# Kernel tuning notes

Measured on AMD Instinct MI355X. Metric: run time of the kernel, lower is better.

Reference implementation:

```python
import jax, jax.numpy as jnp
import numpy as np

EPS = 1e-12  # F.normalize default eps


def _unfold3(x):
    # torch F.unfold(kernel=3, padding=1): [B,C,H,W] -> [B, C*9, H*W],
    # patch elements ordered (c, kh, kw), locations row-major.
    B, C, H, W = x.shape
    xp = jnp.pad(x, ((0, 0), (0, 0), (1, 1), (1, 1)))
    patches = jnp.stack([xp[:, :, i:i + H, j:j + W]
                         for i in range(3) for j in range(3)], axis=2)  # [B,C,9,H,W]
    return patches.reshape(B, C * 9, H * W)


def _fold3(u, H, W):
    # torch F.fold(kernel=3, padding=1): sum of overlapping patches.
    B, CK, L = u.shape
    C = CK // 9
    p = u.reshape(B, C, 3, 3, H, W)
    out = jnp.zeros((B, C, H + 2, W + 2), u.dtype)
    for i in range(3):
        for j in range(3):
            out = out.at[:, :, i:i + H, j:j + W].add(p[:, :, i, j])
    return out[:, :, 1:H + 1, 1:W + 1]


def _l2norm(x, axis):
    n = jnp.sqrt(jnp.sum(x * x, axis=axis, keepdims=True))
    return x / jnp.maximum(n, EPS)


def setup_inputs() -> dict:
    key = jax.random.key(0)
    k1, k2, k3 = jax.random.split(key, 3)
    shape = (4, 256, 64, 64)
    return {
        "feature_current": jax.random.normal(k1, shape, dtype=jnp.float32),
        "feature_refer": jax.random.normal(k2, shape, dtype=jnp.float32),
        "feature_refer_blur": jax.random.normal(k3, shape, dtype=jnp.float32),
    }


def reference(feature_current, feature_refer, feature_refer_blur):
    B, C, H, W = feature_current.shape
    cu = _unfold3(feature_current)                      # [B, C*9, L]
    ru = _unfold3(feature_refer)                        # [B, C*9, L]
    rbu = jnp.transpose(_unfold3(feature_refer_blur), (0, 2, 1))  # [B, L, C*9]
    rbu = _l2norm(rbu, axis=2)
    cu_n = _l2norm(cu, axis=1)
    # cosine similarity between every refer-blur patch and every current patch
    rel = jnp.einsum('bld,bdm->blm', rbu, cu_n)         # [B, L, L]
    max_index = jnp.argmax(rel, axis=1)                 # [B, L] best refer patch per current loc
    # gather matched sharp-reference patches (index broadcast over patch dim)
    matched = jnp.take_along_axis(ru, max_index[:, None, :], axis=2)  # [B, C*9, L]
    folded = _fold3(matched, H, W)                      # [B, C, H, W]
    return feature_current + folded
```

## Files before the change

kernel.cpp:

```cpp
#include <hip/hip_runtime.h>
#include <hip/hip_bf16.h>
#include <stdint.h>

#define HW 4096
#define C_ 256
#define B_ 4

static const size_t CHW = (size_t)C_ * HW;

typedef _Float16 f16;
typedef f16 f16x8 __attribute__((ext_vector_type(8)));
typedef float f32x4 __attribute__((ext_vector_type(4)));

__device__ __forceinline__ unsigned long long pack_key(float v, int i) {
    unsigned u = __float_as_uint(v);
    u = (u & 0x80000000u) ? ~u : (u | 0x80000000u);
    return ((unsigned long long)u << 32) | (unsigned long long)(0xFFFFFFFFu - (unsigned)i);
}

__global__ __launch_bounds__(256) void sqsum_kernel(const float* __restrict__ frb,
                                                    float* __restrict__ sbuf) {
    int b = blockIdx.x;
    int ij = blockIdx.y * 256 + threadIdx.x;
    int g = blockIdx.z;
    const float* p = frb + (size_t)b * CHW + (size_t)g * 32 * HW + ij;
    float s = 0.f;
#pragma unroll 8
    for (int c = 0; c < 32; ++c) {
        float v = p[(size_t)c * HW];
        s = fmaf(v, v, s);
    }
    sbuf[((size_t)b * 8 + g) * HW + ij] = s;
}

__global__ __launch_bounds__(256) void invn_kernel(const float* __restrict__ sbuf,
                                                   float* __restrict__ invn) {
    int b = blockIdx.x;
    int l = blockIdx.y * 256 + threadIdx.x;
    int lh = l >> 6, lw = l & 63;
    float s = 0.f;
#pragma unroll
    for (int dh = -1; dh <= 1; ++dh) {
        int h = lh + dh;
        if ((unsigned)h >= 64u) continue;
#pragma unroll
        for (int dw = -1; dw <= 1; ++dw) {
            int w = lw + dw;
            if ((unsigned)w >= 64u) continue;
            float t = 0.f;
#pragma unroll
            for (int g = 0; g < 8; ++g)
                t += sbuf[((size_t)b * 8 + g) * HW + h * 64 + w];
            s += t;
        }
    }
    float n = sqrtf(s);
    invn[b * HW + l] = 1.0f / fmaxf(n, 1e-12f);
}

__global__ __launch_bounds__(256) void conv_kernel(const float* __restrict__ fcB,
                                                   const float* __restrict__ frbB,
                                                   f16* __restrict__ AB) {
    int zz = blockIdx.z;
    int b = zz >> 1;
    const float* src = ((zz & 1) ? frbB : fcB) + (size_t)b * CHW;
    f16* dst = AB + (size_t)b * 4194304 + (size_t)(zz & 1) * 2097152;
    __shared__ float T[64][65];
    int m0 = blockIdx.x * 64, k0 = blockIdx.y * 64;
    int t = threadIdx.x;
    int kl = t >> 4, mq = (t & 15) * 4;
#pragma unroll
    for (int it = 0; it < 4; ++it) {
        float4 v = *reinterpret_cast<const float4*>(src + (size_t)(k0 + kl + it * 16) * HW + m0 + mq);
        T[kl + it * 16][mq + 0] = v.x;
        T[kl + it * 16][mq + 1] = v.y;
        T[kl + it * 16][mq + 2] = v.z;
        T[kl + it * 16][mq + 3] = v.w;
    }
    __syncthreads();
    int ml = t >> 2, kc = (t & 3) * 16;
    f16x8 h0, h1, lo0, lo1;
#pragma unroll
    for (int j = 0; j < 8; ++j) {
        float a = T[kc + j][ml];
        f16 h = (f16)a;
        h0[j] = h;
        lo0[j] = (f16)(a - (float)h);
        float a2 = T[kc + 8 + j][ml];
        f16 h2 = (f16)a2;
        h1[j] = h2;
        lo1[j] = (f16)(a2 - (float)h2);
    }
    size_t base = (size_t)(m0 + ml) * 512 + k0 + kc;
    *reinterpret_cast<f16x8*>(dst + base) = h0;
    *reinterpret_cast<f16x8*>(dst + base + 8) = h1;
    *reinterpret_cast<f16x8*>(dst + base + 256) = lo0;
    *reinterpret_cast<f16x8*>(dst + base + 264) = lo1;
}

__global__ __launch_bounds__(256, 4) void gram_mfma_kernel(const f16* __restrict__ ABbase,
                                                           float* __restrict__ Gbase) {
    const f16* Af = ABbase + (size_t)blockIdx.z * 4194304;
    const f16* Bf = Af + 2097152;
    float* G = Gbase + (size_t)blockIdx.z * ((size_t)HW * HW);
    __shared__ char Asb[2][16384];
    __shared__ char Bsb[2][16384];
    int tid = threadIdx.x;
    int lane = tid & 63;
    int wave = tid >> 6;
    int wr = wave >> 1, wc = wave & 1;

    int id = blockIdx.y * gridDim.x + blockIdx.x;
    int xcd = id & 7, local = id >> 3;
    int bx = (xcd & 1) * 16 + (local & 15);
    int by = (xcd >> 1) * 8 + (local >> 4);
    int m0 = by * 128, l0 = bx * 128;
    f32x4 acc[4][4] = {};

    int mB = tid >> 3;
    int sw = ((tid & 7) ^ (mB & 7)) << 4;
    const char* gaA0 = (const char*)Af + (size_t)(m0 + mB) * 1024 + sw;
    const char* gaB0 = (const char*)Bf + (size_t)(l0 + mB) * 1024 + sw;
    char* ldA = &Asb[0][0] + (tid & ~63) * 16;
    char* ldB = &Bsb[0][0] + (tid & ~63) * 16;

    unsigned aoff[4], boff[4], choff[2];
#pragma unroll
    for (int q = 0; q < 4; ++q) {
        aoff[q] = (unsigned)((wr * 64 + q * 16 + (lane & 15)) * 128);
        boff[q] = (unsigned)((wc * 64 + q * 16 + (lane & 15)) * 128);
    }
#pragma unroll
    for (int kk = 0; kk < 2; ++kk)
        choff[kk] = (unsigned)((((kk * 4) + (lane >> 4)) ^ (lane & 7)) << 4);

    const int akbArr[12] = {0, 128, 256, 384, 512, 640, 768, 896, 0, 128, 256, 384};
    const int bkbArr[12] = {0, 128, 256, 384, 0, 128, 256, 384, 512, 640, 768, 896};

#define STAGE_TILE(buf, akb, bkb)                                                      \
    {                                                                                  \
        _Pragma("unroll")                                                              \
        for (int i = 0; i < 4; ++i) {                                                  \
            __builtin_amdgcn_global_load_lds(                                          \
                (const __attribute__((address_space(1))) uint32_t*)(gaA0 + i * 32768 + (akb)), \
                (__attribute__((address_space(3))) uint32_t*)(ldA + (buf) * 16384 + i * 4096), \
                16, 0, 0);                                                             \
            __builtin_amdgcn_global_load_lds(                                          \
                (const __attribute__((address_space(1))) uint32_t*)(gaB0 + i * 32768 + (bkb)), \
                (__attribute__((address_space(3))) uint32_t*)(ldB + (buf) * 16384 + i * 4096), \
                16, 0, 0);                                                             \
        }                                                                              \
    }

    STAGE_TILE(0, akbArr[0], bkbArr[0]);
    asm volatile("s_waitcnt vmcnt(0)" ::: "memory");
    __builtin_amdgcn_s_barrier();

#pragma unroll
    for (int t = 0; t < 12; ++t) {
        const int cur = t & 1;
        if (t < 11) STAGE_TILE(cur ^ 1, akbArr[t + 1], bkbArr[t + 1]);
#pragma unroll
        for (int kk = 0; kk < 2; ++kk) {
            f16x8 av[4], bv[4];
#pragma unroll
            for (int q = 0; q < 4; ++q) {
                av[q] = *reinterpret_cast<const f16x8*>(&Asb[cur][0] + aoff[q] + choff[kk]);
                bv[q] = *reinterpret_cast<const f16x8*>(&Bsb[cur][0] + boff[q] + choff[kk]);
            }
#pragma unroll
            for (int mi = 0; mi < 4; ++mi)
#pragma unroll
                for (int ni = 0; ni < 4; ++ni)
                    acc[mi][ni] = __builtin_amdgcn_mfma_f32_16x16x32_f16(
                        av[mi], bv[ni], acc[mi][ni], 0, 0, 0);
        }
        asm volatile("s_waitcnt vmcnt(0)" ::: "memory");
        __builtin_amdgcn_s_barrier();
    }
#undef STAGE_TILE

#pragma unroll
    for (int mi = 0; mi < 4; ++mi) {
#pragma unroll
        for (int ni = 0; ni < 4; ++ni) {
            int n = l0 + wc * 64 + ni * 16 + (lane & 15);
            int mr = m0 + wr * 64 + mi * 16 + (lane >> 4) * 4;
#pragma unroll
            for (int r = 0; r < 4; ++r)
                G[(size_t)(mr + r) * HW + n] = acc[mi][ni][r];
        }
    }
}

#define TBK 32
__global__ __launch_bounds__(256) void gram_kernel(const float* __restrict__ Amat,
                                                   const float* __restrict__ Bmat,
                                                   float* __restrict__ G,
                                                   int l_start, int CWP) {
    __shared__ float As[TBK][128];
    __shared__ float Bs[TBK][128];
    int m0 = blockIdx.y * 128;
    int l0g = l_start + blockIdx.x * 128;
    bool inrange = (l0g >= 0 && l0g < HW);
    int tid = threadIdx.x;
    int tx = tid & 15;
    int ty = tid >> 4;
    float acc[8][8] = {};

    if (inrange) {
        for (int k0 = 0; k0 < C_; k0 += TBK) {
#pragma unroll
            for (int it = 0; it < 4; ++it) {
                int idx = tid + it * 256;
                int r = idx >> 5;
                int c4 = idx & 31;
                float4 av = *reinterpret_cast<const float4*>(Amat + (size_t)(k0 + r) * HW + m0 + c4 * 4);
                *reinterpret_cast<float4*>(&As[r][c4 * 4]) = av;
                float4 bv = *reinterpret_cast<const float4*>(Bmat + (size_t)(k0 + r) * HW + l0g + c4 * 4);
                *reinterpret_cast<float4*>(&Bs[r][c4 * 4]) = bv;
            }
            __syncthreads();
#pragma unroll
            for (int k = 0; k < TBK; ++k) {
                float a[8], bb[8];
                *(float4*)&a[0] = *(float4*)&As[k][ty * 8];
                *(float4*)&a[4] = *(float4*)&As[k][ty * 8 + 4];
                *(float4*)&bb[0] = *(float4*)&Bs[k][tx * 8];
                *(float4*)&bb[4] = *(float4*)&Bs[k][tx * 8 + 4];
#pragma unroll
                for (int i = 0; i < 8; ++i)
#pragma unroll
                    for (int j = 0; j < 8; ++j)
                        acc[i][j] = fmaf(a[i], bb[j], acc[i][j]);
            }
            __syncthreads();
        }
    }
#pragma unroll
    for (int i = 0; i < 8; ++i) {
        int m = m0 + ty * 8 + i;
        float* row = G + (size_t)m * CWP + blockIdx.x * 128 + tx * 8;
        *(float4*)row = *(float4*)&acc[i][0];
        *(float4*)(row + 4) = *(float4*)&acc[i][4];
    }
}

__global__ __launch_bounds__(512, 4) void argmax3_kernel(const float* __restrict__ Gbase,
                                                         const float* __restrict__ invnB,
                                                         unsigned long long* __restrict__ keysB) {
    const float* G = Gbase + (size_t)blockIdx.z * ((size_t)HW * HW);
    const float* invn = invnB + (size_t)blockIdx.z * HW;
    unsigned long long* keys = keysB + (size_t)blockIdx.z * HW;

    int id = blockIdx.y * gridDim.x + blockIdx.x;
    int xcd = id & 7, pos = id >> 3;
    int mh = xcd * 8 + (pos >> 3);
    int c0 = (pos & 7) * 8;

    int lane = threadIdx.x & 63;
    int wave = threadIdx.x >> 6;
    int mwb = wave * 8;

    bool laneUp = lane >= 1, laneDn = lane <= 62;
    bool mhUp = mh >= 1, mhDn = mh <= 62;

    unsigned rowOff[3][10];
    int br0 = max(mh - 1, 0) * 64, br1 = mh * 64, br2 = min(mh + 1, 63) * 64;
#pragma unroll
    for (int j = 0; j < 10; ++j) {
        int mwr = min(max(mwb - 1 + j, 0), 63);
        rowOff[0][j] = (unsigned)((br0 + mwr) * 4096 + lane);
        rowOff[1][j] = (unsigned)((br1 + mwr) * 4096 + lane);
        rowOff[2][j] = (unsigned)((br2 + mwr) * 4096 + lane);
    }

    float A[8], B[8];
#pragma unroll
    for (int i = 0; i < 8; ++i) { A[i] = 0.f; B[i] = 0.f; }
    float maxv[8];
    int maxi[8];
#pragma unroll
    for (int i = 0; i < 8; ++i) { maxv[i] = -INFINITY; maxi[i] = 0; }
    float invPrev = 0.f;

    for (int c = c0 - 1; c <= c0 + 8; ++c) {
        int cc = min(max(c, 0), 63);
        unsigned colOff = (unsigned)(cc * 64);
        float g[3][10];
#pragma unroll
        for (int b = 0; b < 3; ++b)
#pragma unroll
            for (int j = 0; j < 10; ++j)
                g[b][j] = G[(size_t)(rowOff[b][j] + colOff)];
        float invCur = invn[colOff + lane];

        if (c - 1 >= c0) {
            bool vp = mhDn && (c <= 63);
            int lbase = (c - 1) * 64 + lane;
#pragma unroll
            for (int i = 0; i < 8; ++i) {
                float up = __shfl_up(g[2][i], 1);
                float dn = __shfl_down(g[2][i + 2], 1);
                float w = g[2][i + 1];
                w += (laneUp && (mwb + i >= 1)) ? up : 0.f;
                w += (laneDn && (mwb + i <= 62)) ? dn : 0.f;
                float R = A[i] + (vp ? w : 0.f);
                float score = R * invPrev;
                if (score > maxv[i]) { maxv[i] = score; maxi[i] = lbase; }
            }
        }
        bool vm = mhUp && (c >= 0);
#pragma unroll
        for (int i = 0; i < 8; ++i) {
            float up1 = __shfl_up(g[1][i], 1);
            float dn1 = __shfl_down(g[1][i + 2], 1);
            float w1 = g[1][i + 1];
            w1 += (laneUp && (mwb + i >= 1)) ? up1 : 0.f;
            w1 += (laneDn && (mwb + i <= 62)) ? dn1 : 0.f;
            A[i] = B[i] + w1;

            float up0 = __shfl_up(g[0][i], 1);
            float dn0 = __shfl_down(g[0][i + 2], 1);
            float w0 = g[0][i + 1];
            w0 += (laneUp && (mwb + i >= 1)) ? up0 : 0.f;
            w0 += (laneDn && (mwb + i <= 62)) ? dn0 : 0.f;
            B[i] = vm ? w0 : 0.f;
        }
        invPrev = invCur;
    }

#pragma unroll
    for (int i = 0; i < 8; ++i) {
        float v = maxv[i];
        int idx = maxi[i];
#pragma unroll
        for (int off = 32; off >= 1; off >>= 1) {
            float v2 = __shfl_xor(v, off);
            int i2 = __shfl_xor(idx, off);
            if (v2 > v || (v2 == v && i2 < idx)) { v = v2; idx = i2; }
        }
        if (lane == 0) atomicMax(&keys[mh * 64 + mwb + i], pack_key(v, idx));
    }
}

__global__ __launch_bounds__(512, 8) void argmax_kernel(const float* __restrict__ Gbase,
                                                        const float* __restrict__ invnB,
                                                        unsigned long long* __restrict__ keysB,
                                                        int lh0, int l_start, int CWP) {
    const float* G = Gbase;
    const float* invn = invnB;
    unsigned long long* keys = keysB;
    int mh = blockIdx.x;
    int lh_base = lh0 + blockIdx.y * 4;
    int wave = threadIdx.x >> 6;
    int lane = threadIdx.x & 63;
    int mwbase = wave * 8;

    float maxv[8];
    int maxi[8];
#pragma unroll
    for (int i = 0; i < 8; ++i) { maxv[i] = -INFINITY; maxi[i] = 0; }

    for (int lhs = 0; lhs < 4; ++lhs) {
        int lh = lh_base + lhs;
        int l = lh * 64 + lane;
        float inv = invn[l];
        float R[8];
#pragma unroll
        for (int i = 0; i < 8; ++i) R[i] = 0.f;

#pragma unroll
        for (int dh = -1; dh <= 1; ++dh) {
            if ((unsigned)(mh + dh) >= 64u || (unsigned)(lh + dh) >= 64u) continue;
            const float* Gb = G + (size_t)((mh + dh) * 64) * CWP + ((lh + dh) * 64 - l_start) + lane;
            float v[10];
#pragma unroll
            for (int j = 0; j < 10; ++j) {
                int mw2 = mwbase - 1 + j;
                int mwc = min(max(mw2, 0), 63);
                float tv = Gb[(size_t)mwc * CWP];
                v[j] = ((unsigned)mw2 < 64u) ? tv : 0.f;
            }
#pragma unroll
            for (int mi = 0; mi < 8; ++mi) {
                float a = __shfl_up(v[mi], 1);
                float c = __shfl_down(v[mi + 2], 1);
                float s = v[mi + 1];
                s += (lane > 0) ? a : 0.f;
                s += (lane < 63) ? c : 0.f;
                R[mi] += s;
            }
        }
#pragma unroll
        for (int mi = 0; mi < 8; ++mi) {
            float score = R[mi] * inv;
            if (score > maxv[mi]) { maxv[mi] = score; maxi[mi] = l; }
        }
    }

#pragma unroll
    for (int mi = 0; mi < 8; ++mi) {
        float v = maxv[mi];
        int idx = maxi[mi];
#pragma unroll
        for (int off = 32; off >= 1; off >>= 1) {
            float v2 = __shfl_xor(v, off);
            int i2 = __shfl_xor(idx, off);
            if (v2 > v || (v2 == v && i2 < idx)) { v = v2; idx = i2; }
        }
        if (lane == 0) {
            int m = mh * 64 + mwbase + mi;
            atomicMax(&keys[m], pack_key(v, idx));
        }
    }
}

__global__ __launch_bounds__(256) void fold_kernel(const float* __restrict__ fc,
                                                   const float* __restrict__ fr,
                                                   const unsigned long long* __restrict__ keys,
                                                   float* __restrict__ out) {
    int b = blockIdx.y;
    int c0 = blockIdx.x * 2;
    __shared__ float frL[2 * 4096];
    __shared__ int idxL[4096];
    int t = threadIdx.x;

    const float* fsrc = fr + (size_t)b * CHW + (size_t)c0 * HW;
#pragma unroll
    for (int it = 0; it < 8; ++it) {
        int o = (it * 256 + t) * 4;
        *reinterpret_cast<float4*>(&frL[o]) = *reinterpret_cast<const float4*>(&fsrc[o]);
    }
#pragma unroll
    for (int it = 0; it < 16; ++it) {
        int m = it * 256 + t;
        unsigned long long kk = keys[(size_t)b * HW + m];
        idxL[m] = (int)(0xFFFFFFFFu - (unsigned)(kk & 0xFFFFFFFFull));
    }
    __syncthreads();

    int j = t & 63, w = t >> 6;
    int c = c0 + (w & 1);
    int i0 = (w >> 1) * 32;
    const float* frowL = &frL[(w & 1) * 4096];
    const float* fcrow = fc + (size_t)b * CHW + (size_t)c * HW;
    float* orow = out + (size_t)b * CHW + (size_t)c * HW;

    for (int i = i0; i < i0 + 32; ++i) {
        float acc = fcrow[i * 64 + j];
#pragma unroll
        for (int kh = 0; kh < 3; ++kh) {
            int mhp = i + 1 - kh;
            if ((unsigned)mhp >= 64u) continue;
#pragma unroll
            for (int kw = 0; kw < 3; ++kw) {
                int mwp = j + 1 - kw;
                float contrib = 0.f;
                if ((unsigned)mwp < 64u) {
                    int idx = idxL[mhp * 64 + mwp];
                    int sh = (idx >> 6) + kh - 1;
                    int sw = (idx & 63) + kw - 1;
                    if ((unsigned)sh < 64u && (unsigned)sw < 64u)
                        contrib = frowL[sh * 64 + sw];
                }
                acc += contrib;
            }
        }
        orow[i * 64 + j] = acc;
    }
}

extern "C" void kernel_launch(void* const* d_in, const int* in_sizes, int n_in,
                              void* d_out, int out_size, void* d_ws, size_t ws_size,
                              hipStream_t stream) {
    const float* fc = (const float*)d_in[0];
    const float* fr = (const float*)d_in[1];
    const float* frb = (const float*)d_in[2];
    float* out = (float*)d_out;

    char* ws = (char*)d_ws;
    unsigned long long* keys = (unsigned long long*)ws;
    float* invn = (float*)(ws + 131072);
    float* sbuf = (float*)(ws + 196608);
    const size_t HDR = 720896;

    size_t abBytes = (size_t)2 * HW * 512 * sizeof(f16);
    size_t gBytes = (size_t)HW * HW * 4;
    size_t needB = HDR + 4 * abBytes + gBytes;
    size_t needC = HDR + abBytes + gBytes;

    hipMemsetAsync(keys, 0, 131072, stream);
    sqsum_kernel<<<dim3(B_, 16, 8), 256, 0, stream>>>(frb, sbuf);
    invn_kernel<<<dim3(B_, 16), 256, 0, stream>>>(sbuf, invn);

    if (ws_size >= needC) {
        bool mergedConv = (ws_size >= needB);
        int nab = mergedConv ? 4 : 1;
        f16* AB = (f16*)(ws + HDR);
        float* G = (float*)(ws + HDR + (size_t)nab * abBytes);

        if (mergedConv)
            conv_kernel<<<dim3(64, 4, 8), 256, 0, stream>>>(fc, frb, AB);

        for (int b = 0; b < B_; ++b) {
            if (!mergedConv)
                conv_kernel<<<dim3(64, 4, 2), 256, 0, stream>>>(
                    fc + (size_t)b * CHW, frb + (size_t)b * CHW, AB);
            f16* ABslot = AB + (size_t)(mergedConv ? b : 0) * 4194304;
            gram_mfma_kernel<<<dim3(32, 32, 1), 256, 0, stream>>>(ABslot, G);
            argmax3_kernel<<<dim3(64, 8, 1), 512, 0, stream>>>(
                G, invn + (size_t)b * HW, keys + (size_t)b * HW);
        }
    } else {
        float* G = (float*)(ws + HDR);
        int CW = 4096, PAD = 0;
        while (CW >= 256) {
            PAD = (CW == 4096) ? 0 : 128;
            size_t need = HDR + (size_t)HW * (CW + 2 * PAD) * 4;
            if (need <= ws_size) break;
            CW >>= 1;
        }
        int CWP = CW + 2 * PAD;
        for (int b = 0; b < B_; ++b) {
            for (int cb = 0; cb < HW; cb += CW) {
                int l_start = cb - PAD;
                gram_kernel<<<dim3(CWP / 128, 32), 256, 0, stream>>>(
                    fc + (size_t)b * CHW, frb + (size_t)b * CHW, G, l_start, CWP);
                argmax_kernel<<<dim3(64, CW / 256, 1), 512, 0, stream>>>(
                    G, invn + (size_t)b * HW, keys + (size_t)b * HW,
                    cb / 64, l_start, CWP);
            }
        }
    }
    fold_kernel<<<dim3(128, B_), 256, 0, stream>>>(fc, fr, keys, out);
}
```

Before: 305.6 us.

## Replace 128x128 gram MFMA kernel with 256x256 tile, 8-wave pipelined kernel

Swaps the 128x128-tile, 4-wave gram GEMM for a 256x256-tile kernel with 8 waves and 128KB of dynamic LDS. Each K-slab is split into halves and loads are interleaved with MFMA phases behind barriers and partial vmcnt waits. It also raises wave priority around the MFMA blocks. The larger tile doubles operand reuse per LDS byte, and the finer staging is meant to hide global-to-LDS latency. In exchange it raises register pressure (32 accumulators per lane), adds many barriers, and launches only 256 blocks per batch, which may underfill the GPU.

```diff
diff --git a/kernel.cpp b/kernel.cpp
--- a/kernel.cpp
+++ b/kernel.cpp
@@ -11,6 +11,10 @@
 typedef _Float16 f16;
 typedef f16 f16x8 __attribute__((ext_vector_type(8)));
 typedef float f32x4 __attribute__((ext_vector_type(4)));
+
+#define AS1 __attribute__((address_space(1)))
+#define AS3 __attribute__((address_space(3)))
+#define GLL(src, dst) __builtin_amdgcn_global_load_lds((const AS1 uint32_t*)(src), (AS3 uint32_t*)(dst), 16, 0, 0)
 
 __device__ __forceinline__ unsigned long long pack_key(float v, int i) {
     unsigned u = __float_as_uint(v);
@@ -98,94 +102,146 @@
     *reinterpret_cast<f16x8*>(dst + base + 264) = lo1;
 }
 
-__global__ __launch_bounds__(256, 4) void gram_mfma_kernel(const f16* __restrict__ ABbase,
-                                                           float* __restrict__ Gbase) {
-    const f16* Af = ABbase + (size_t)blockIdx.z * 4194304;
+__global__ __launch_bounds__(512, 2) void gram256_kernel(const f16* __restrict__ ABbase,
+                                                         float* __restrict__ Gbase) {
+    extern __shared__ char lds[];
+    char* ldsA = lds;
+    char* ldsB = lds + 65536;
+    const f16* Af = ABbase;
     const f16* Bf = Af + 2097152;
-    float* G = Gbase + (size_t)blockIdx.z * ((size_t)HW * HW);
-    __shared__ char Asb[2][16384];
-    __shared__ char Bsb[2][16384];
+    float* G = Gbase;
+
     int tid = threadIdx.x;
     int lane = tid & 63;
     int wave = tid >> 6;
-    int wr = wave >> 1, wc = wave & 1;
-
-    int id = blockIdx.y * gridDim.x + blockIdx.x;
+    int wr = wave >> 2, wc = wave & 3;
+
+    int id = blockIdx.y * 16 + blockIdx.x;
     int xcd = id & 7, local = id >> 3;
-    int bx = (xcd & 1) * 16 + (local & 15);
-    int by = (xcd >> 1) * 8 + (local >> 4);
-    int m0 = by * 128, l0 = bx * 128;
-    f32x4 acc[4][4] = {};
-
-    int mB = tid >> 3;
-    int sw = ((tid & 7) ^ (mB & 7)) << 4;
-    const char* gaA0 = (const char*)Af + (size_t)(m0 + mB) * 1024 + sw;
-    const char* gaB0 = (const char*)Bf + (size_t)(l0 + mB) * 1024 + sw;
-    char* ldA = &Asb[0][0] + (tid & ~63) * 16;
-    char* ldB = &Bsb[0][0] + (tid & ~63) * 16;
-
-    unsigned aoff[4], boff[4], choff[2];
-#pragma unroll
-    for (int q = 0; q < 4; ++q) {
-        aoff[q] = (unsigned)((wr * 64 + q * 16 + (lane & 15)) * 128);
-        boff[q] = (unsigned)((wc * 64 + q * 16 + (lane & 15)) * 128);
-    }
-#pragma unroll
-    for (int kk = 0; kk < 2; ++kk)
-        choff[kk] = (unsigned)((((kk * 4) + (lane >> 4)) ^ (lane & 7)) << 4);
+    int bx = (xcd & 1) * 8 + (local & 7);
+    int by = (xcd >> 1) * 4 + (local >> 3);
+    int m0 = by * 256, l0 = bx * 256;
+
+    f32x4 acc[8][4] = {};
+
+    int r0 = tid >> 2, s0 = tid & 3;
+    const char* sA0 = (const char*)Af + (size_t)(m0 + r0) * 1024 + ((s0 ^ (r0 & 3)) << 4);
+    const char* sB0 = (const char*)Bf + (size_t)(l0 + r0) * 1024 + ((s0 ^ (r0 & 3)) << 4);
+    unsigned wbase = (unsigned)(tid & ~63) * 16;
+
+#define STAGE_A(su, h, kb)                                                       \
+    do {                                                                         \
+        GLL(sA0 + (kb) + (h) * 64, ldsA + (su) * 32768 + (h) * 16384 + wbase);   \
+        GLL(sA0 + 131072 + (kb) + (h) * 64,                                      \
+            ldsA + (su) * 32768 + (h) * 16384 + wbase + 8192);                   \
+    } while (0)
+#define STAGE_B(su, h, kb)                                                       \
+    do {                                                                         \
+        GLL(sB0 + (kb) + (h) * 64, ldsB + (su) * 32768 + (h) * 16384 + wbase);   \
+        GLL(sB0 + 131072 + (kb) + (h) * 64,                                      \
+            ldsB + (su) * 32768 + (h) * 16384 + wbase + 8192);                   \
+    } while (0)
+
+    unsigned rsw = (unsigned)(((lane >> 4) ^ (lane & 3)) << 4);
+    unsigned aRow = (unsigned)((wr * 128 + (lane & 15)) * 64) + rsw;
+    unsigned bRow = (unsigned)((wc * 64 + (lane & 15)) * 64) + rsw;
 
     const int akbArr[12] = {0, 128, 256, 384, 512, 640, 768, 896, 0, 128, 256, 384};
     const int bkbArr[12] = {0, 128, 256, 384, 0, 128, 256, 384, 512, 640, 768, 896};
 
-#define STAGE_TILE(buf, akb, bkb)                                                      \
-    {                                                                                  \
-        _Pragma("unroll")                                                              \
-        for (int i = 0; i < 4; ++i) {                                                  \
-            __builtin_amdgcn_global_load_lds(                                          \
-                (const __attribute__((address_space(1))) uint32_t*)(gaA0 + i * 32768 + (akb)), \
-                (__attribute__((address_space(3))) uint32_t*)(ldA + (buf) * 16384 + i * 4096), \
-                16, 0, 0);                                                             \
-            __builtin_amdgcn_global_load_lds(                                          \
-                (const __attribute__((address_space(1))) uint32_t*)(gaB0 + i * 32768 + (bkb)), \
-                (__attribute__((address_space(3))) uint32_t*)(ldB + (buf) * 16384 + i * 4096), \
-                16, 0, 0);                                                             \
-        }                                                                              \
-    }
-
-    STAGE_TILE(0, akbArr[0], bkbArr[0]);
+    STAGE_A(0, 0, akbArr[0]);
+    STAGE_B(0, 0, bkbArr[0]);
+    STAGE_A(0, 1, akbArr[0]);
+    STAGE_B(0, 1, bkbArr[0]);
     asm volatile("s_waitcnt vmcnt(0)" ::: "memory");
     __builtin_amdgcn_s_barrier();
 
+    f16x8 av[4], bv[4];
 #pragma unroll
     for (int t = 0; t < 12; ++t) {
-        const int cur = t & 1;
-        if (t < 11) STAGE_TILE(cur ^ 1, akbArr[t + 1], bkbArr[t + 1]);
-#pragma unroll
-        for (int kk = 0; kk < 2; ++kk) {
-            f16x8 av[4], bv[4];
-#pragma unroll
-            for (int q = 0; q < 4; ++q) {
-                av[q] = *reinterpret_cast<const f16x8*>(&Asb[cur][0] + aoff[q] + choff[kk]);
-                bv[q] = *reinterpret_cast<const f16x8*>(&Bsb[cur][0] + boff[q] + choff[kk]);
-            }
-#pragma unroll
-            for (int mi = 0; mi < 4; ++mi)
-#pragma unroll
-                for (int ni = 0; ni < 4; ++ni)
-                    acc[mi][ni] = __builtin_amdgcn_mfma_f32_16x16x32_f16(
-                        av[mi], bv[ni], acc[mi][ni], 0, 0, 0);
-        }
-        asm volatile("s_waitcnt vmcnt(0)" ::: "memory");
-        __builtin_amdgcn_s_barrier();
-    }
-#undef STAGE_TILE
-
-#pragma unroll
-    for (int mi = 0; mi < 4; ++mi) {
+        const int slot = t & 1, su = slot ^ 1;
+        const bool pf = (t < 11);
+        const int akbN = pf ? akbArr[t + 1] : 0;
+        const int bkbN = pf ? bkbArr[t + 1] : 0;
+        const char* Ab0 = ldsA + slot * 32768;
+        const char* Bb0 = ldsB + slot * 32768;
+        const char* Ab1 = Ab0 + 16384;
+        const char* Bb1 = Bb0 + 16384;
+
+#pragma unroll
+        for (int ni = 0; ni < 4; ++ni)
+            bv[ni] = *reinterpret_cast<const f16x8*>(Bb0 + bRow + ni * 1024);
+#pragma unroll
+        for (int q = 0; q < 4; ++q)
+            av[q] = *reinterpret_cast<const f16x8*>(Ab0 + aRow + q * 1024);
+        if (pf) STAGE_A(su, 0, akbN);
+        __builtin_amdgcn_s_barrier();
+        __builtin_amdgcn_s_setprio(1);
+#pragma unroll
+        for (int q = 0; q < 4; ++q)
+#pragma unroll
+            for (int ni = 0; ni < 4; ++ni)
+                acc[q][ni] = __builtin_amdgcn_mfma_f32_16x16x32_f16(av[q], bv[ni], acc[q][ni], 0, 0, 0);
+        __builtin_amdgcn_s_setprio(0);
+        __builtin_amdgcn_s_barrier();
+
+#pragma unroll
+        for (int q = 0; q < 4; ++q)
+            av[q] = *reinterpret_cast<const f16x8*>(Ab0 + aRow + 4096 + q * 1024);
+        if (pf) STAGE_B(su, 0, bkbN);
+        __builtin_amdgcn_s_barrier();
+        __builtin_amdgcn_s_setprio(1);
+#pragma unroll
+        for (int q = 0; q < 4; ++q)
+#pragma unroll
+            for (int ni = 0; ni < 4; ++ni)
+                acc[4 + q][ni] = __builtin_amdgcn_mfma_f32_16x16x32_f16(av[q], bv[ni], acc[4 + q][ni], 0, 0, 0);
+        __builtin_amdgcn_s_setprio(0);
+        if (t < 11) asm volatile("s_waitcnt vmcnt(4)" ::: "memory");
+        else        asm volatile("s_waitcnt vmcnt(0)" ::: "memory");
+        __builtin_amdgcn_s_barrier();
+
+#pragma unroll
+        for (int ni = 0; ni < 4; ++ni)
+            bv[ni] = *reinterpret_cast<const f16x8*>(Bb1 + bRow + ni * 1024);
+#pragma unroll
+        for (int q = 0; q < 4; ++q)
+            av[q] = *reinterpret_cast<const f16x8*>(Ab1 + aRow + q * 1024);
+        if (pf) STAGE_A(su, 1, akbN);
+        __builtin_amdgcn_s_barrier();
+        __builtin_amdgcn_s_setprio(1);
+#pragma unroll
+        for (int q = 0; q < 4; ++q)
+#pragma unroll
+            for (int ni = 0; ni < 4; ++ni)
+                acc[q][ni] = __builtin_amdgcn_mfma_f32_16x16x32_f16(av[q], bv[ni], acc[q][ni], 0, 0, 0);
+        __builtin_amdgcn_s_setprio(0);
+        __builtin_amdgcn_s_barrier();
+
+#pragma unroll
+        for (int q = 0; q < 4; ++q)
+            av[q] = *reinterpret_cast<const f16x8*>(Ab1 + aRow + 4096 + q * 1024);
+        if (pf) STAGE_B(su, 1, bkbN);
+        __builtin_amdgcn_s_barrier();
+        __builtin_amdgcn_s_setprio(1);
+#pragma unroll
+        for (int q = 0; q < 4; ++q)
+#pragma unroll
+            for (int ni = 0; ni < 4; ++ni)
+                acc[4 + q][ni] = __builtin_amdgcn_mfma_f32_16x16x32_f16(av[q], bv[ni], acc[4 + q][ni], 0, 0, 0);
+        __builtin_amdgcn_s_setprio(0);
+        if (t < 11) asm volatile("s_waitcnt vmcnt(4)" ::: "memory");
+        __builtin_amdgcn_s_barrier();
+    }
+#undef STAGE_A
+#undef STAGE_B
+
+#pragma unroll
+    for (int mi = 0; mi < 8; ++mi) {
 #pragma unroll
         for (int ni = 0; ni < 4; ++ni) {
             int n = l0 + wc * 64 + ni * 16 + (lane & 15);
-            int mr = m0 + wr * 64 + mi * 16 + (lane >> 4) * 4;
+            int mr = m0 + wr * 128 + mi * 16 + (lane >> 4) * 4;
 #pragma unroll
             for (int r = 0; r < 4; ++r)
                 G[(size_t)(mr + r) * HW + n] = acc[mi][ni][r];
@@ -500,6 +556,9 @@
         f16* AB = (f16*)(ws + HDR);
         float* G = (float*)(ws + HDR + (size_t)nab * abBytes);
 
+        hipFuncSetAttribute(reinterpret_cast<const void*>(&gram256_kernel),
+                            hipFuncAttributeMaxDynamicSharedMemorySize, 131072);
+
         if (mergedConv)
             conv_kernel<<<dim3(64, 4, 8), 256, 0, stream>>>(fc, frb, AB);
 
@@ -508,7 +567,7 @@
                 conv_kernel<<<dim3(64, 4, 2), 256, 0, stream>>>(
                     fc + (size_t)b * CHW, frb + (size_t)b * CHW, AB);
             f16* ABslot = AB + (size_t)(mergedConv ? b : 0) * 4194304;
-            gram_mfma_kernel<<<dim3(32, 32, 1), 256, 0, stream>>>(ABslot, G);
+            gram256_kernel<<<dim3(16, 16, 1), 512, 131072, stream>>>(ABslot, G);
             argmax3_kernel<<<dim3(64, 8, 1), 512, 0, stream>>>(
                 G, invn + (size_t)b * HW, keys + (size_t)b * HW);
         }
```

Measured after the change: 308.5 us. About the same (+1.0%).
